# Kernel optimization log

Hardware: AMD Instinct MI355X
Metric: run time of the kernel (lower is better)

The kernel has to match this reference:

```python
import jax, jax.numpy as jnp
import numpy as np

N_NODES = 100000
N_EDGES = 1200000
IN_CH, HID_CH, OUT_CH = 64, 64, 32


def setup_inputs() -> dict:
    key = jax.random.key(0)
    ks = jax.random.split(key, 8)
    x = jax.random.normal(ks[0], (N_NODES, IN_CH), dtype=jnp.float32)
    edge_index = jax.random.randint(ks[1], (2, N_EDGES), 0, N_NODES, dtype=jnp.int64)
    # SAGEConv params: lin_l acts on aggregated neighbors (has bias), lin_r on root features.
    def glorot(k, fan_in, fan_out):
        s = jnp.sqrt(6.0 / (fan_in + fan_out))
        return jax.random.uniform(k, (fan_in, fan_out), jnp.float32, -s, s)
    W1_l = glorot(ks[2], IN_CH, HID_CH)
    W1_r = glorot(ks[3], IN_CH, HID_CH)
    b1 = jnp.zeros((HID_CH,), jnp.float32)
    W2_l = glorot(ks[4], HID_CH, OUT_CH)
    W2_r = glorot(ks[5], HID_CH, OUT_CH)
    b2 = jnp.zeros((OUT_CH,), jnp.float32)
    return {"x": x, "edge_index": edge_index, "W1_l": W1_l, "W1_r": W1_r,
            "b1": b1, "W2_l": W2_l, "W2_r": W2_r, "b2": b2}


def _sage_conv(h, src, dst, W_l, W_r, b):
    # gather source-node features along edges, mean-aggregate at destinations
    msg = h[src]                                               # [E, d]
    agg = jax.ops.segment_sum(msg, dst, num_segments=N_NODES)  # [N, d]
    cnt = jax.ops.segment_sum(jnp.ones((msg.shape[0],), h.dtype), dst,
                              num_segments=N_NODES)
    agg = agg / jnp.maximum(cnt, 1.0)[:, None]                 # mean (0 if no neighbors)
    return agg @ W_l + h @ W_r + b


def reference(x, edge_index, W1_l, W1_r, b1, W2_l, W2_r, b2):
    src, dst = edge_index[0], edge_index[1]
    h = _sage_conv(x, src, dst, W1_l, W1_r, b1)
    h = jax.nn.relu(h)
    # dropout is identity in eval mode
    return _sage_conv(h, src, dst, W2_l, W2_r, b2)
```

## Files before the change

### kernel.cpp

```cpp
#include <hip/hip_runtime.h>

__device__ __forceinline__ float bf2f(unsigned short u) {
    union { unsigned int i; float f; } v;
    v.i = ((unsigned int)u) << 16;
    return v.f;
}
__device__ __forceinline__ unsigned short f2bf(float f) {
    union { float f; unsigned int u; } v;
    v.f = f;
    unsigned int u = v.u;
    u += 0x7FFFu + ((u >> 16) & 1u);
    return (unsigned short)(u >> 16);
}
__device__ __forceinline__ unsigned int pack2bf(float lo, float hi) {
    return (unsigned int)f2bf(lo) | ((unsigned int)f2bf(hi) << 16);
}
__device__ __forceinline__ float loadElem(const void* p, size_t i, int isb) {
    return isb ? bf2f(((const unsigned short*)p)[i]) : ((const float*)p)[i];
}
__device__ __forceinline__ float bflo(unsigned int u) {
    union { unsigned int i; float f; } v; v.i = u << 16; return v.f;
}
__device__ __forceinline__ float bfhi(unsigned int u) {
    union { unsigned int i; float f; } v; v.i = u & 0xFFFF0000u; return v.f;
}

typedef __attribute__((ext_vector_type(8))) short bf16x8;
typedef __attribute__((ext_vector_type(4))) float f32x4;

#define CHUNK 4096
#define BSHIFT 8

__device__ __forceinline__ void detect_local(
        const int* ei, int nd, const unsigned int* xw, int nxw,
        int* sh, int& q, int& isb) {
    int t = threadIdx.x;
    int v = 0;
    for (int i = 1 + 2 * t; i < nd; i += 512) v |= ei[i];
    int pl = 0;
    for (int i = t; i < nxw; i += 256) {
        unsigned short lo = (unsigned short)(xw[i] & 0xFFFFu);
        float a = fabsf(bf2f(lo));
        if (a > 1e-5f && a < 100.0f) pl++;
    }
    sh[t] = v; sh[256 + t] = pl;
    __syncthreads();
    for (int off = 128; off > 0; off >>= 1) {
        if (t < off) { sh[t] |= sh[t + off]; sh[256 + t] += sh[256 + t + off]; }
        __syncthreads();
    }
    q   = (sh[0] == 0) ? 1 : 0;
    isb = (2 * sh[256] >= nxw) ? 1 : 0;
    __syncthreads();
}

__global__ __launch_bounds__(256) void k_prep(
        const int* __restrict__ ei, const void* __restrict__ x,
        int* __restrict__ blockHist, unsigned short* __restrict__ xb,
        const void* __restrict__ W1l, const void* __restrict__ W1r,
        const void* __restrict__ b1,
        const void* __restrict__ W2l, const void* __restrict__ W2r,
        const void* __restrict__ b2,
        unsigned short* __restrict__ wt1l, unsigned short* __restrict__ wt1r,
        unsigned short* __restrict__ wt2lr,
        float* __restrict__ bs1, float* __restrict__ bs2,
        int E, int NBUK, int nblk, int n8, int nd, int nxw) {
    __shared__ int sh[768];
    int t = threadIdx.x;
    int b = blockIdx.x;
    int q, isb;
    detect_local(ei, nd, (const unsigned int*)x, nxw, sh, q, isb);

    for (int i = t; i < NBUK; i += 256) sh[i] = 0;
    __syncthreads();
    int e0 = b * CHUNK, e1 = min(E, e0 + CHUNK);
    for (int e = e0 + t; e < e1; e += 256) {
        int dst = ei[((size_t)(E + e)) << q];
        atomicAdd(&sh[dst >> BSHIFT], 1);
    }
    __syncthreads();
    for (int i = t; i < NBUK; i += 256)
        blockHist[(size_t)i * nblk + b] = sh[i];

    if (b == 0) {
        for (int i = t; i < 64 * 64; i += 256) {
            int c = i >> 6, k = i & 63;
            wt1l[c * 72 + k] = isb ? ((const unsigned short*)W1l)[k * 64 + c]
                                   : f2bf(((const float*)W1l)[k * 64 + c]);
        }
    } else if (b == 1) {
        for (int i = t; i < 64 * 64; i += 256) {
            int c = i >> 6, k = i & 63;
            wt1r[c * 72 + k] = isb ? ((const unsigned short*)W1r)[k * 64 + c]
                                   : f2bf(((const float*)W1r)[k * 64 + c]);
        }
    } else if (b == 2) {
        for (int i = t; i < 32 * 64; i += 256) {
            int c = i >> 6, k = i & 63;
            wt2lr[c * 72 + k]        = isb ? ((const unsigned short*)W2l)[k * 32 + c]
                                           : f2bf(((const float*)W2l)[k * 32 + c]);
            wt2lr[(32 + c) * 72 + k] = isb ? ((const unsigned short*)W2r)[k * 32 + c]
                                           : f2bf(((const float*)W2r)[k * 32 + c]);
        }
        if (t < 64) bs1[t] = loadElem(b1, t, isb);
        if (t >= 64 && t < 96) bs2[t - 64] = loadElem(b2, t - 64, isb);
    }

    for (int i = b * 256 + t; i < n8; i += gridDim.x * 256) {
        if (isb) {
            ((uint4*)xb)[i] = ((const uint4*)x)[i];
        } else {
            const float4* xf = (const float4*)x;
            float4 p = xf[2 * i], r = xf[2 * i + 1];
            ushort4 lo = { f2bf(p.x), f2bf(p.y), f2bf(p.z), f2bf(p.w) };
            ushort4 hi = { f2bf(r.x), f2bf(r.y), f2bf(r.z), f2bf(r.w) };
            ((ushort4*)xb)[2 * i] = lo;
            ((ushort4*)xb)[2 * i + 1] = hi;
        }
    }
}

__global__ __launch_bounds__(256) void k_rowscan(
        int* __restrict__ blockHist, int* __restrict__ bukTot, int nblk) {
    __shared__ int sh[256];
    int t = threadIdx.x;
    int* row = blockHist + (size_t)blockIdx.x * nblk;
    int carry = 0;
    for (int base = 0; base < nblk; base += 256) {
        int i = base + t;
        int v = (i < nblk) ? row[i] : 0;
        sh[t] = v;
        __syncthreads();
        for (int off = 1; off < 256; off <<= 1) {
            int u = (t >= off) ? sh[t - off] : 0;
            __syncthreads();
            sh[t] += u;
            __syncthreads();
        }
        if (i < nblk) row[i] = carry + sh[t] - v;
        int tot = sh[255];
        __syncthreads();
        carry += tot;
    }
    if (t == 0) bukTot[blockIdx.x] = carry;
}

__global__ __launch_bounds__(512) void k_toto(
        const int* __restrict__ bukTot, int* __restrict__ bukOff,
        int* __restrict__ rowptr, int NBUK, int E, int N) {
    __shared__ int sh[512];
    int t = threadIdx.x;
    int v = (t < NBUK) ? bukTot[t] : 0;
    sh[t] = v;
    __syncthreads();
    for (int off = 1; off < 512; off <<= 1) {
        int u = (t >= off) ? sh[t - off] : 0;
        __syncthreads();
        sh[t] += u;
        __syncthreads();
    }
    if (t < NBUK) bukOff[t] = sh[t] - v;
    if (t == 0) { bukOff[NBUK] = E; rowptr[N] = E; }
}

__global__ __launch_bounds__(256) void k_part(
        const int* __restrict__ ei,
        const int* __restrict__ blockHist, const int* __restrict__ bukOff,
        unsigned int* __restrict__ recs, int E, int NBUK, int nblk, int nd) {
    __shared__ int sh[768];
    int t = threadIdx.x;
    int q, isb;
    detect_local(ei, nd, (const unsigned int*)ei, 0, sh, q, isb);
    for (int i = t; i < NBUK; i += 256)
        sh[i] = blockHist[(size_t)i * nblk + blockIdx.x] + bukOff[i];
    __syncthreads();
    int e0 = blockIdx.x * CHUNK, e1 = min(E, e0 + CHUNK);
    for (int e = e0 + t; e < e1; e += 256) {
        int dst = ei[((size_t)(E + e)) << q];
        int src = ei[((size_t)e) << q];
        int pos = atomicAdd(&sh[dst >> BSHIFT], 1);
        recs[pos] = ((unsigned int)src << BSHIFT) | (unsigned int)(dst & ((1 << BSHIFT) - 1));
    }
}

__global__ __launch_bounds__(256) void k_csr(
        const unsigned int* __restrict__ recs, const int* __restrict__ bukOff,
        int* __restrict__ rowptr, int* __restrict__ esorted, int N) {
    __shared__ int degLoc[256];
    __shared__ int offLoc[256];
    __shared__ int wcur[256];
    int t = threadIdx.x;
    int node0 = blockIdx.x << BSHIFT;
    int r0 = bukOff[blockIdx.x], r1 = bukOff[blockIdx.x + 1];
    degLoc[t] = 0;
    __syncthreads();
    for (int i = r0 + t; i < r1; i += 256)
        atomicAdd(&degLoc[recs[i] & 255], 1);
    __syncthreads();
    int v = degLoc[t];
    offLoc[t] = v;
    __syncthreads();
    for (int off = 1; off < 256; off <<= 1) {
        int u = (t >= off) ? offLoc[t - off] : 0;
        __syncthreads();
        offLoc[t] += u;
        __syncthreads();
    }
    int excl = offLoc[t] - v;
    int node = node0 + t;
    if (node < N) rowptr[node] = r0 + excl;
    wcur[t] = r0 + excl;
    __syncthreads();
    for (int i = r0 + t; i < r1; i += 256) {
        unsigned int rec = recs[i];
        int pos = atomicAdd(&wcur[rec & 255], 1);
        esorted[pos] = (int)(rec >> BSHIFT);
    }
}

__global__ __launch_bounds__(256) void k_fused1(
        const unsigned short* __restrict__ feat,
        const int* __restrict__ rowptr,
        const int* __restrict__ esorted,
        const unsigned short* __restrict__ wt1l,
        const unsigned short* __restrict__ wt1r,
        const unsigned short* __restrict__ wt2lr,
        const float* __restrict__ bs1,
        const float* __restrict__ bs2,
        unsigned short* __restrict__ zbuf,
        unsigned short* __restrict__ gbuf,
        int N) {
    constexpr int SA2 = 72;
    constexpr int SW  = 72;
    __shared__ __align__(16) unsigned short amB16[64 * SA2];
    __shared__ __align__(16) unsigned short wT[64 * SW];
    __shared__ float Bs[64];
    __shared__ float Bs2[32];

    int t = threadIdx.x;
    int node0 = blockIdx.x << 6;

    for (int i = t; i < 576; i += 256)
        ((uint4*)wT)[i] = ((const uint4*)wt1l)[i];
    if (t < 64) Bs[t] = bs1[t];
    if (t >= 64 && t < 96) Bs2[t - 64] = bs2[t - 64];

    {
        int g = t >> 3, l = t & 7;
        const unsigned short* fl = feat + 8 * l;
#pragma unroll
        for (int jj = 0; jj < 2; ++jj) {
            int nl = g + 32 * jj;
            int node = node0 + nl;
            float a0 = 0.f, a1 = 0.f, a2 = 0.f, a3 = 0.f;
            float a4 = 0.f, a5 = 0.f, a6 = 0.f, a7 = 0.f;
            float inv = 0.f;
            if (node < N) {
                int beg = rowptr[node], end = rowptr[node + 1];
                int d = end - beg;
                if (d > 0) {
                    inv = 1.0f / (float)d;
                    for (int bs = beg; bs < end; bs += 8) {
                        int cnt = min(end - bs, 8);
                        const int* ep = esorted + bs;
                        int dd = 0;
                        if (cnt == 8) {
                            int s0 = ep[0], s1 = ep[1], s2 = ep[2], s3 = ep[3];
                            int s4 = ep[4], s5 = ep[5], s6 = ep[6], s7 = ep[7];
                            uint4 u0 = *(const uint4*)(fl + (size_t)s0 * 64);
                            uint4 u1 = *(const uint4*)(fl + (size_t)s1 * 64);
                            uint4 u2 = *(const uint4*)(fl + (size_t)s2 * 64);
                            uint4 u3 = *(const uint4*)(fl + (size_t)s3 * 64);
                            uint4 u4 = *(const uint4*)(fl + (size_t)s4 * 64);
                            uint4 u5 = *(const uint4*)(fl + (size_t)s5 * 64);
                            uint4 u6 = *(const uint4*)(fl + (size_t)s6 * 64);
                            uint4 u7 = *(const uint4*)(fl + (size_t)s7 * 64);
                            a0 += bflo(u0.x) + bflo(u1.x) + bflo(u2.x) + bflo(u3.x)
                                + bflo(u4.x) + bflo(u5.x) + bflo(u6.x) + bflo(u7.x);
                            a1 += bfhi(u0.x) + bfhi(u1.x) + bfhi(u2.x) + bfhi(u3.x)
                                + bfhi(u4.x) + bfhi(u5.x) + bfhi(u6.x) + bfhi(u7.x);
                            a2 += bflo(u0.y) + bflo(u1.y) + bflo(u2.y) + bflo(u3.y)
                                + bflo(u4.y) + bflo(u5.y) + bflo(u6.y) + bflo(u7.y);
                            a3 += bfhi(u0.y) + bfhi(u1.y) + bfhi(u2.y) + bfhi(u3.y)
                                + bfhi(u4.y) + bfhi(u5.y) + bfhi(u6.y) + bfhi(u7.y);
                            a4 += bflo(u0.z) + bflo(u1.z) + bflo(u2.z) + bflo(u3.z)
                                + bflo(u4.z) + bflo(u5.z) + bflo(u6.z) + bflo(u7.z);
                            a5 += bfhi(u0.z) + bfhi(u1.z) + bfhi(u2.z) + bfhi(u3.z)
                                + bfhi(u4.z) + bfhi(u5.z) + bfhi(u6.z) + bfhi(u7.z);
                            a6 += bflo(u0.w) + bflo(u1.w) + bflo(u2.w) + bflo(u3.w)
                                + bflo(u4.w) + bflo(u5.w) + bflo(u6.w) + bflo(u7.w);
                            a7 += bfhi(u0.w) + bfhi(u1.w) + bfhi(u2.w) + bfhi(u3.w)
                                + bfhi(u4.w) + bfhi(u5.w) + bfhi(u6.w) + bfhi(u7.w);
                            dd = 8;
                        }
                        for (; dd + 4 <= cnt; dd += 4) {
                            int s0 = ep[dd + 0], s1 = ep[dd + 1];
                            int s2 = ep[dd + 2], s3 = ep[dd + 3];
                            uint4 u0 = *(const uint4*)(fl + (size_t)s0 * 64);
                            uint4 u1 = *(const uint4*)(fl + (size_t)s1 * 64);
                            uint4 u2 = *(const uint4*)(fl + (size_t)s2 * 64);
                            uint4 u3 = *(const uint4*)(fl + (size_t)s3 * 64);
                            a0 += bflo(u0.x) + bflo(u1.x) + bflo(u2.x) + bflo(u3.x);
                            a1 += bfhi(u0.x) + bfhi(u1.x) + bfhi(u2.x) + bfhi(u3.x);
                            a2 += bflo(u0.y) + bflo(u1.y) + bflo(u2.y) + bflo(u3.y);
                            a3 += bfhi(u0.y) + bfhi(u1.y) + bfhi(u2.y) + bfhi(u3.y);
                            a4 += bflo(u0.z) + bflo(u1.z) + bflo(u2.z) + bflo(u3.z);
                            a5 += bfhi(u0.z) + bfhi(u1.z) + bfhi(u2.z) + bfhi(u3.z);
                            a6 += bflo(u0.w) + bflo(u1.w) + bflo(u2.w) + bflo(u3.w);
                            a7 += bfhi(u0.w) + bfhi(u1.w) + bfhi(u2.w) + bfhi(u3.w);
                        }
                        for (; dd < cnt; ++dd) {
                            int s = ep[dd];
                            uint4 u = *(const uint4*)(fl + (size_t)s * 64);
                            a0 += bflo(u.x); a1 += bfhi(u.x);
                            a2 += bflo(u.y); a3 += bfhi(u.y);
                            a4 += bflo(u.z); a5 += bfhi(u.z);
                            a6 += bflo(u.w); a7 += bfhi(u.w);
                        }
                    }
                }
            }
            uint4 packed = make_uint4(pack2bf(a0 * inv, a1 * inv),
                                      pack2bf(a2 * inv, a3 * inv),
                                      pack2bf(a4 * inv, a5 * inv),
                                      pack2bf(a6 * inv, a7 * inv));
            *(uint4*)&amB16[nl * SA2 + 8 * l] = packed;
        }
    }
    __syncthreads();

    int wid = t >> 6, lane = t & 63;
    int arow = lane & 15;
    int kgrp = (lane >> 4) * 8;
    f32x4 acc[4];
#pragma unroll
    for (int ct = 0; ct < 4; ++ct) acc[ct] = (f32x4){0.f, 0.f, 0.f, 0.f};

    const unsigned short* aBase = &amB16[(16 * wid + arow) * SA2 + kgrp];
#pragma unroll
    for (int kh = 0; kh < 2; ++kh) {
        bf16x8 a = *(const bf16x8*)(aBase + kh * 32);
#pragma unroll
        for (int ct = 0; ct < 4; ++ct) {
            bf16x8 bb = *(const bf16x8*)&wT[(16 * ct + arow) * SW + kh * 32 + kgrp];
            acc[ct] = __builtin_amdgcn_mfma_f32_16x16x32_bf16(a, bb, acc[ct], 0, 0, 0);
        }
    }
    __syncthreads();

    for (int i = t; i < 64 * 8; i += 256) {
        int nl = i >> 3, c = i & 7;
        int gn = node0 + nl;
        uint4 u = make_uint4(0u, 0u, 0u, 0u);
        if (gn < N) u = *(const uint4*)(feat + (size_t)gn * 64 + 8 * c);
        *(uint4*)&amB16[nl * SA2 + 8 * c] = u;
    }
    for (int i = t; i < 576; i += 256)
        ((uint4*)wT)[i] = ((const uint4*)wt1r)[i];
    __syncthreads();

#pragma unroll
    for (int kh = 0; kh < 2; ++kh) {
        bf16x8 a = *(const bf16x8*)(aBase + kh * 32);
#pragma unroll
        for (int ct = 0; ct < 4; ++ct) {
            bf16x8 bb = *(const bf16x8*)&wT[(16 * ct + arow) * SW + kh * 32 + kgrp];
            acc[ct] = __builtin_amdgcn_mfma_f32_16x16x32_bf16(a, bb, acc[ct], 0, 0, 0);
        }
    }
    __syncthreads();

    {
        int rbase = (lane >> 4) * 4;
#pragma unroll
        for (int ct = 0; ct < 4; ++ct) {
            int ch = 16 * ct + arow;
            float bv = Bs[ch];
#pragma unroll
            for (int r = 0; r < 4; ++r) {
                int nl = 16 * wid + rbase + r;
                float v = fmaxf(acc[ct][r] + bv, 0.f);
                amB16[nl * SA2 + ch] = f2bf(v);
            }
        }
    }
    for (int i = t; i < 576; i += 256)
        ((uint4*)wT)[i] = ((const uint4*)wt2lr)[i];
    __syncthreads();

    f32x4 accz[2], accg[2];
#pragma unroll
    for (int ct = 0; ct < 2; ++ct) {
        accz[ct] = (f32x4){0.f, 0.f, 0.f, 0.f};
        accg[ct] = (f32x4){0.f, 0.f, 0.f, 0.f};
    }
#pragma unroll
    for (int kh = 0; kh < 2; ++kh) {
        bf16x8 a = *(const bf16x8*)(aBase + kh * 32);
#pragma unroll
        for (int ct = 0; ct < 2; ++ct) {
            bf16x8 bz = *(const bf16x8*)&wT[(16 * ct + arow) * SW + kh * 32 + kgrp];
            bf16x8 bg = *(const bf16x8*)&wT[(32 + 16 * ct + arow) * SW + kh * 32 + kgrp];
            accz[ct] = __builtin_amdgcn_mfma_f32_16x16x32_bf16(a, bz, accz[ct], 0, 0, 0);
            accg[ct] = __builtin_amdgcn_mfma_f32_16x16x32_bf16(a, bg, accg[ct], 0, 0, 0);
        }
    }

#pragma unroll
    for (int ct = 0; ct < 2; ++ct) {
        int ch = 16 * ct + arow;
        float b2v = Bs2[ch];
#pragma unroll
        for (int r = 0; r < 4; ++r) {
            int node = node0 + 16 * wid + (lane >> 4) * 4 + r;
            if (node >= N) continue;
            zbuf[(size_t)node * 32 + ch] = f2bf(accz[ct][r]);
            gbuf[(size_t)node * 32 + ch] = f2bf(accg[ct][r] + b2v);
        }
    }
}

__global__ __launch_bounds__(256) void k_final(
        const unsigned short* __restrict__ zbuf,
        const unsigned short* __restrict__ gbuf,
        const int* __restrict__ rowptr,
        const int* __restrict__ esorted,
        void* __restrict__ outp,
        int N, const void* __restrict__ x, int nxw) {
    __shared__ int shp[256];
    int t = threadIdx.x;
    int node0 = blockIdx.x << 6;

    {
        const unsigned int* xw = (const unsigned int*)x;
        int pl = 0;
        for (int i = t; i < nxw; i += 256) {
            unsigned short lo = (unsigned short)(xw[i] & 0xFFFFu);
            float a = fabsf(bf2f(lo));
            if (a > 1e-5f && a < 100.0f) pl++;
        }
        shp[t] = pl;
        __syncthreads();
        for (int off = 128; off > 0; off >>= 1) {
            if (t < off) shp[t] += shp[t + off];
            __syncthreads();
        }
    }
    int isb = (2 * shp[0] >= nxw) ? 1 : 0;

    int g = t >> 3, l = t & 7;
    const unsigned short* fl = zbuf + 4 * l;
#pragma unroll
    for (int jj = 0; jj < 2; ++jj) {
        int nl = g + 32 * jj;
        int node = node0 + nl;
        if (node >= N) continue;
        float a0 = 0.f, a1 = 0.f, a2 = 0.f, a3 = 0.f;
        float inv = 0.f;
        int beg = rowptr[node], end = rowptr[node + 1];
        int d = end - beg;
        if (d > 0) {
            inv = 1.0f / (float)d;
            for (int bs = beg; bs < end; bs += 8) {
                int cnt = min(end - bs, 8);
                const int* ep = esorted + bs;
                int dd = 0;
                if (cnt == 8) {
                    int s0 = ep[0], s1 = ep[1], s2 = ep[2], s3 = ep[3];
                    int s4 = ep[4], s5 = ep[5], s6 = ep[6], s7 = ep[7];
                    uint2 u0 = *(const uint2*)(fl + (size_t)s0 * 32);
                    uint2 u1 = *(const uint2*)(fl + (size_t)s1 * 32);
                    uint2 u2 = *(const uint2*)(fl + (size_t)s2 * 32);
                    uint2 u3 = *(const uint2*)(fl + (size_t)s3 * 32);
                    uint2 u4 = *(const uint2*)(fl + (size_t)s4 * 32);
                    uint2 u5 = *(const uint2*)(fl + (size_t)s5 * 32);
                    uint2 u6 = *(const uint2*)(fl + (size_t)s6 * 32);
                    uint2 u7 = *(const uint2*)(fl + (size_t)s7 * 32);
                    a0 += bflo(u0.x) + bflo(u1.x) + bflo(u2.x) + bflo(u3.x)
                        + bflo(u4.x) + bflo(u5.x) + bflo(u6.x) + bflo(u7.x);
                    a1 += bfhi(u0.x) + bfhi(u1.x) + bfhi(u2.x) + bfhi(u3.x)
                        + bfhi(u4.x) + bfhi(u5.x) + bfhi(u6.x) + bfhi(u7.x);
                    a2 += bflo(u0.y) + bflo(u1.y) + bflo(u2.y) + bflo(u3.y)
                        + bflo(u4.y) + bflo(u5.y) + bflo(u6.y) + bflo(u7.y);
                    a3 += bfhi(u0.y) + bfhi(u1.y) + bfhi(u2.y) + bfhi(u3.y)
                        + bfhi(u4.y) + bfhi(u5.y) + bfhi(u6.y) + bfhi(u7.y);
                    dd = 8;
                }
                for (; dd + 4 <= cnt; dd += 4) {
                    int s0 = ep[dd + 0], s1 = ep[dd + 1];
                    int s2 = ep[dd + 2], s3 = ep[dd + 3];
                    uint2 u0 = *(const uint2*)(fl + (size_t)s0 * 32);
                    uint2 u1 = *(const uint2*)(fl + (size_t)s1 * 32);
                    uint2 u2 = *(const uint2*)(fl + (size_t)s2 * 32);
                    uint2 u3 = *(const uint2*)(fl + (size_t)s3 * 32);
                    a0 += bflo(u0.x) + bflo(u1.x) + bflo(u2.x) + bflo(u3.x);
                    a1 += bfhi(u0.x) + bfhi(u1.x) + bfhi(u2.x) + bfhi(u3.x);
                    a2 += bflo(u0.y) + bflo(u1.y) + bflo(u2.y) + bflo(u3.y);
                    a3 += bfhi(u0.y) + bfhi(u1.y) + bfhi(u2.y) + bfhi(u3.y);
                }
                for (; dd < cnt; ++dd) {
                    int s = ep[dd];
                    uint2 u = *(const uint2*)(fl + (size_t)s * 32);
                    a0 += bflo(u.x); a1 += bfhi(u.x);
                    a2 += bflo(u.y); a3 += bfhi(u.y);
                }
            }
        }
        uint2 gv = *(const uint2*)(gbuf + (size_t)node * 32 + 4 * l);
        float r0 = a0 * inv + bflo(gv.x);
        float r1 = a1 * inv + bfhi(gv.x);
        float r2 = a2 * inv + bflo(gv.y);
        float r3 = a3 * inv + bfhi(gv.y);
        if (!isb) {
            *(float4*)((float*)outp + (size_t)node * 32 + 4 * l) =
                make_float4(r0, r1, r2, r3);
        } else {
            ushort4 o = { f2bf(r0), f2bf(r1), f2bf(r2), f2bf(r3) };
            *(ushort4*)((unsigned short*)outp + (size_t)node * 32 + 4 * l) = o;
        }
    }
}

extern "C" void kernel_launch(void* const* d_in, const int* in_sizes, int n_in,
                              void* d_out, int out_size, void* d_ws, size_t ws_size,
                              hipStream_t stream) {
    const void* x   = d_in[0];
    const int*  ei  = (const int*)d_in[1];
    const void* W1l = d_in[2];
    const void* W1r = d_in[3];
    const void* b1  = d_in[4];
    const void* W2l = d_in[5];
    const void* W2r = d_in[6];
    const void* b2  = d_in[7];

    const int N = in_sizes[0] / 64;
    const int E = in_sizes[1] / 2;
    const int NBUK = (N + (1 << BSHIFT) - 1) >> BSHIFT;
    const int nblk = (E + CHUNK - 1) / CHUNK;

    char* base = (char*)d_ws;
    size_t off = 0;
    auto alloc = [&](size_t bytes) { size_t o = off; off = (off + bytes + 255) & ~(size_t)255; return o; };
    int* bukTot  = (int*)(base + alloc((size_t)NBUK * 4));
    int* bukOff  = (int*)(base + alloc((size_t)(NBUK + 1) * 4));
    int* rowptr  = (int*)(base + alloc((size_t)(N + 1) * 4));
    unsigned int* recs = (unsigned int*)(base + alloc((size_t)E * 4));
    int* esorted = (int*)(base + alloc((size_t)E * 4));
    unsigned short* xb = (unsigned short*)(base + alloc((size_t)N * 64 * 2));
    unsigned short* h  = (unsigned short*)(base + alloc((size_t)N * 64 * 2));
    unsigned short* wt1l  = (unsigned short*)(base + alloc(64 * 72 * 2));
    unsigned short* wt1r  = (unsigned short*)(base + alloc(64 * 72 * 2));
    unsigned short* wt2lr = (unsigned short*)(base + alloc(64 * 72 * 2));
    float* bs1 = (float*)(base + alloc(64 * 4));
    float* bs2 = (float*)(base + alloc(32 * 4));
    int* blockHist = (int*)(base + alloc((size_t)NBUK * nblk * 4));
    (void)ws_size;

    unsigned short* zbuf = h;
    unsigned short* gbuf = h + (size_t)N * 32;

    int nd = 2 * E; if (nd > 2048) nd = 2048;
    const int nxw = 512;

    k_prep<<<nblk, 256, 0, stream>>>(ei, x, blockHist, xb,
                                     W1l, W1r, b1, W2l, W2r, b2,
                                     wt1l, wt1r, wt2lr, bs1, bs2,
                                     E, NBUK, nblk, N * 8, nd, nxw);
    k_rowscan<<<NBUK, 256, 0, stream>>>(blockHist, bukTot, nblk);
    k_toto<<<1, 512, 0, stream>>>(bukTot, bukOff, rowptr, NBUK, E, N);
    k_part<<<nblk, 256, 0, stream>>>(ei, blockHist, bukOff, recs, E, NBUK, nblk, nd);
    k_csr<<<NBUK, 256, 0, stream>>>(recs, bukOff, rowptr, esorted, N);

    const int ntile = (N + 63) / 64;
    k_fused1<<<ntile, 256, 0, stream>>>(xb, rowptr, esorted,
                                        wt1l, wt1r, wt2lr, bs1, bs2,
                                        zbuf, gbuf, N);
    k_final<<<ntile, 256, 0, stream>>>(zbuf, gbuf, rowptr, esorted, d_out, N, x, nxw);
}
```

Baseline: 206.2 us.

## Stage partition records in shared memory for coalesced bucket-ordered writes

Measured after the change: 208.4 us. About the same (+1.1%).

```diff
diff --git a/kernel.cpp b/kernel.cpp
--- a/kernel.cpp
+++ b/kernel.cpp
@@ -167,20 +167,64 @@
         const int* __restrict__ ei,
         const int* __restrict__ blockHist, const int* __restrict__ bukOff,
         unsigned int* __restrict__ recs, int E, int NBUK, int nblk, int nd) {
-    __shared__ int sh[768];
-    int t = threadIdx.x;
+    __shared__ int sh[512];
+    __shared__ int cnt[512];
+    __shared__ int pre[512];
+    __shared__ int outb[512];
+    __shared__ unsigned int srec[CHUNK];
+    __shared__ unsigned short sbuk[CHUNK];
+    int t = threadIdx.x;
+    int b = blockIdx.x;
     int q, isb;
     detect_local(ei, nd, (const unsigned int*)ei, 0, sh, q, isb);
+
+    for (int i = t; i < NBUK; i += 256) cnt[i] = 0;
+    __syncthreads();
+
+    int e0 = b * CHUNK, e1 = min(E, e0 + CHUNK);
+    for (int e = e0 + t; e < e1; e += 256) {
+        int dst = ei[((size_t)(E + e)) << q];
+        atomicAdd(&cnt[dst >> BSHIFT], 1);
+    }
+    __syncthreads();
+
+    int carry = 0;
+    for (int base = 0; base < NBUK; base += 256) {
+        int i = base + t;
+        int v = (i < NBUK) ? cnt[i] : 0;
+        sh[t] = v;
+        __syncthreads();
+        for (int off = 1; off < 256; off <<= 1) {
+            int u = (t >= off) ? sh[t - off] : 0;
+            __syncthreads();
+            sh[t] += u;
+            __syncthreads();
+        }
+        if (i < NBUK) pre[i] = carry + sh[t] - v;
+        int tot = sh[255];
+        __syncthreads();
+        carry += tot;
+    }
+
     for (int i = t; i < NBUK; i += 256)
-        sh[i] = blockHist[(size_t)i * nblk + blockIdx.x] + bukOff[i];
-    __syncthreads();
-    int e0 = blockIdx.x * CHUNK, e1 = min(E, e0 + CHUNK);
+        outb[i] = bukOff[i] + blockHist[(size_t)i * nblk + b] - pre[i];
+    __syncthreads();
+    for (int i = t; i < NBUK; i += 256) cnt[i] = pre[i];
+    __syncthreads();
+
     for (int e = e0 + t; e < e1; e += 256) {
         int dst = ei[((size_t)(E + e)) << q];
         int src = ei[((size_t)e) << q];
-        int pos = atomicAdd(&sh[dst >> BSHIFT], 1);
-        recs[pos] = ((unsigned int)src << BSHIFT) | (unsigned int)(dst & ((1 << BSHIFT) - 1));
-    }
+        int bk = dst >> BSHIFT;
+        int p = atomicAdd(&cnt[bk], 1);
+        srec[p] = ((unsigned int)src << BSHIFT) | (unsigned int)(dst & ((1 << BSHIFT) - 1));
+        sbuk[p] = (unsigned short)bk;
+    }
+    __syncthreads();
+
+    int n = e1 - e0;
+    for (int p = t; p < n; p += 256)
+        recs[outb[sbuk[p]] + p] = srec[p];
 }
 
 __global__ __launch_bounds__(256) void k_csr(
```
